# Kernel tuning notes

Hardware: AMD Instinct MI355X
Metric: run time of the kernel (lower is better)

The kernel has to match this reference:

```python
import jax, jax.numpy as jnp
import numpy as np

B, N, D, H = 8, 4096, 1024, 16
HD = D // H
EPS = 1e-5  # torch layer_norm default


def setup_inputs() -> dict:
    key = jax.random.key(0)
    ks = jax.random.split(key, 18)
    s = 1.0 / np.sqrt(D)

    def lin(k):
        return jax.random.normal(k, (D, D), jnp.float32) * s, jnp.zeros((D,), jnp.float32)

    Wg_w, Wg_b = lin(ks[0])
    Wr_w, Wr_b = lin(ks[1])
    Wk_w, Wk_b = lin(ks[2])
    Wv_w, Wv_b = lin(ks[3])
    Wo_w, Wo_b = lin(ks[4])
    mg = jax.random.uniform(ks[5], (D,), jnp.float32)
    mr = jax.random.uniform(ks[6], (D,), jnp.float32)
    mk = jax.random.uniform(ks[7], (D,), jnp.float32)
    mv = jax.random.uniform(ks[8], (D,), jnp.float32)
    w = jax.random.normal(ks[9], (H, HD), jnp.float32)
    u = jax.random.normal(ks[10], (H, HD), jnp.float32)
    x = jax.random.normal(ks[11], (B, N, D), jnp.float32)
    return {"x": x, "Wg_w": Wg_w, "Wg_b": Wg_b, "Wr_w": Wr_w, "Wr_b": Wr_b,
            "Wk_w": Wk_w, "Wk_b": Wk_b, "Wv_w": Wv_w, "Wv_b": Wv_b,
            "Wo_w": Wo_w, "Wo_b": Wo_b, "mg": mg, "mr": mr, "mk": mk, "mv": mv,
            "w": w, "u": u}


def reference(x, Wg_w, Wg_b, Wr_w, Wr_b, Wk_w, Wk_b, Wv_w, Wv_b, Wo_w, Wo_b,
              mg, mr, mk, mv, w, u):
    b, n, d = x.shape
    x_shift = jnp.roll(x, shift=1, axis=1)  # torch.roll wraps: row 0 <- row N-1

    def mix(m, W, bias):
        return (m * x + (1.0 - m) * x_shift) @ W.T + bias

    g = mix(mg, Wg_w, Wg_b).reshape(b, n, H, HD)
    r = mix(mr, Wr_w, Wr_b).reshape(b, n, H, HD)
    k = mix(mk, Wk_w, Wk_b).reshape(b, n, H, HD)
    v = mix(mv, Wv_w, Wv_b).reshape(b, n, H, HD)

    kv = k * v  # [B,N,H,HD]
    decay = jnp.exp(-jnp.exp(w))  # [H,HD]

    # sequential decay scan over time: acc_t = decay*acc_{t-1} + kv_t
    kv_t = jnp.swapaxes(kv, 0, 1)  # [N,B,H,HD]

    def step(acc, kvt):
        acc = decay * acc + kvt
        return acc, acc

    _, accs = jax.lax.scan(step, jnp.zeros((b, H, HD), x.dtype), kv_t)
    wkv = jnp.swapaxes(accs, 0, 1) + u * kv  # [B,N,H,HD]

    rw = r * wkv
    mean = jnp.mean(rw, axis=-1, keepdims=True)
    var = jnp.var(rw, axis=-1, keepdims=True)
    ln = (rw - mean) * jax.lax.rsqrt(var + EPS)

    out = (jax.nn.sigmoid(g) * ln).reshape(b, n, d)
    return out @ Wo_w.T + Wo_b
```

## Files before the change

### kernel.cpp

```cpp
#include <hip/hip_runtime.h>
#include <stdint.h>

#define NB 8
#define NSEQ 4096
#define DMODEL 1024
#define NH 16
#define HDIM 64
#define MROWS (NB*NSEQ)
#define NCHUNK 128
#define CHUNKL (NSEQ/NCHUNK)
#define MIXROWS 16

typedef unsigned short u16;
typedef float f32x4 __attribute__((ext_vector_type(4)));
typedef short bf16x8 __attribute__((ext_vector_type(8)));
typedef unsigned short u16x8 __attribute__((ext_vector_type(8)));

__device__ __forceinline__ u16 f2b(float f) {
  unsigned int u = __builtin_bit_cast(unsigned int, f);
  u = (u + 0x7FFFu + ((u >> 16) & 1u)) >> 16;
  return (u16)u;
}
__device__ __forceinline__ float b2f(u16 s) {
  unsigned int u = ((unsigned int)s) << 16;
  return __builtin_bit_cast(float, u);
}

__device__ __forceinline__ void gload16(const void* g, void* l) {
  __builtin_amdgcn_global_load_lds(
      (const __attribute__((address_space(1))) void*)g,
      (__attribute__((address_space(3))) void*)l, 16, 0, 0);
}

__global__ __launch_bounds__(256) void cvt5(
    const float* __restrict__ a0, const float* __restrict__ a1,
    const float* __restrict__ a2, const float* __restrict__ a3,
    const float* __restrict__ a4,
    u16* __restrict__ b0, u16* __restrict__ b1, u16* __restrict__ b2,
    u16* __restrict__ b3, u16* __restrict__ b4)
{
  const int mat = blockIdx.x >> 7;
  const int blk = blockIdx.x & 127;
  const float* s; u16* d;
  switch (mat) {
    case 0: s = a0; d = b0; break;
    case 1: s = a1; d = b1; break;
    case 2: s = a2; d = b2; break;
    case 3: s = a3; d = b3; break;
    default: s = a4; d = b4; break;
  }
#pragma unroll
  for (int it = 0; it < 8; ++it) {
    const int idx = blk*8192 + it*1024 + threadIdx.x*4;
    const float4 v = *(const float4*)(s + idx);
    ushort4 o; o.x = f2b(v.x); o.y = f2b(v.y); o.z = f2b(v.z); o.w = f2b(v.w);
    *(ushort4*)(d + idx) = o;
  }
}

__global__ __launch_bounds__(256) void mix4_kernel(
    const float* __restrict__ X,
    const float* __restrict__ mg, const float* __restrict__ mr,
    const float* __restrict__ mk, const float* __restrict__ mv,
    u16* __restrict__ Ag, u16* __restrict__ Ar, u16* __restrict__ Ak, u16* __restrict__ Av)
{
  const int g = threadIdx.x >> 7;
  const int t = threadIdx.x & 127;
  const int c8 = t * 8;
  const int r0 = blockIdx.x * MIXROWS + g * (MIXROWS/2);

  float mgv[8], mrv[8], mkv[8], mvv[8];
  *(float4*)&mgv[0] = *(const float4*)(mg + c8); *(float4*)&mgv[4] = *(const float4*)(mg + c8 + 4);
  *(float4*)&mrv[0] = *(const float4*)(mr + c8); *(float4*)&mrv[4] = *(const float4*)(mr + c8 + 4);
  *(float4*)&mkv[0] = *(const float4*)(mk + c8); *(float4*)&mkv[4] = *(const float4*)(mk + c8 + 4);
  *(float4*)&mvv[0] = *(const float4*)(mv + c8); *(float4*)&mvv[4] = *(const float4*)(mv + c8 + 4);

  const int nidx = r0 & (NSEQ-1);
  const int prow = (nidx == 0) ? r0 + (NSEQ-1) : r0 - 1;
  float prev[8];
  *(float4*)&prev[0] = *(const float4*)(X + (size_t)prow*DMODEL + c8);
  *(float4*)&prev[4] = *(const float4*)(X + (size_t)prow*DMODEL + c8 + 4);

#pragma unroll
  for (int j = 0; j < MIXROWS/2; ++j) {
    const size_t o = (size_t)(r0 + j)*DMODEL + c8;
    float cur[8];
    *(float4*)&cur[0] = *(const float4*)(X + o);
    *(float4*)&cur[4] = *(const float4*)(X + o + 4);
#define DO_MIX(MV, AP) { \
      bf16x8 s_; \
      _Pragma("unroll") \
      for (int e = 0; e < 8; ++e) s_[e] = (short)f2b(prev[e] + MV[e]*(cur[e]-prev[e])); \
      *(bf16x8*)(AP + o) = s_; }
    DO_MIX(mgv, Ag)
    DO_MIX(mrv, Ar)
    DO_MIX(mkv, Ak)
    DO_MIX(mvv, Av)
#undef DO_MIX
#pragma unroll
    for (int e = 0; e < 8; ++e) prev[e] = cur[e];
  }
}

#define FENCE asm volatile("" ::: "memory")
#define BAR() { FENCE; __builtin_amdgcn_s_barrier(); FENCE; }
#define PRIO1 __builtin_amdgcn_s_setprio(1)
#define PRIO0 __builtin_amdgcn_s_setprio(0)
#define VM6 asm volatile("s_waitcnt vmcnt(6)" ::: "memory")
#define VM4 asm volatile("s_waitcnt vmcnt(4)" ::: "memory")
#define VM0 asm volatile("s_waitcnt vmcnt(0)" ::: "memory")

template<int OUTBF, int NSEG>
__global__ __launch_bounds__(512, 2) void gemm256(
    const u16* __restrict__ A0, const u16* __restrict__ W0,
    const float* __restrict__ b0, float* __restrict__ oF0, u16* __restrict__ oB0,
    const u16* __restrict__ A1, const u16* __restrict__ W1,
    const float* __restrict__ b1, float* __restrict__ oF1, u16* __restrict__ oB1)
{
  __shared__ __align__(16) char lds[131072];
  const int tid = threadIdx.x;
  const int wave = tid >> 6, lane = tid & 63;
  const int wm = wave >> 2, wn = wave & 3;
  const int rla = lane & 15, kgrp = lane >> 4;

  const int seg = (NSEG == 2) ? (blockIdx.x >> 9) : 0;
  const u16* Abf = (seg == 0) ? A0 : A1;
  const u16* Wb  = (seg == 0) ? W0 : W1;
  const float* bias = (seg == 0) ? b0 : b1;
  float* outF = (seg == 0) ? oF0 : oF1;
  u16*   outB = (seg == 0) ? oB0 : oB1;

  const int wg = blockIdx.x & 511;
  const int xcd = wg & 7, slot = wg >> 3;
  const int by = xcd*16 + (slot >> 2);
  const int bx = slot & 3;

  const int F0 = (wave*2+0)*1024 + lane*16;
  const int F1 = (wave*2+1)*1024 + lane*16;
  const int r0 = F0 >> 6, r1 = F1 >> 6;
  const int c80 = ((F0 >> 4) & 3) ^ ((r0 >> 1) & 3);
  const int c81 = ((F1 >> 4) & 3) ^ ((r1 >> 1) & 3);
  const char* Ab = (const char*)Abf;
  const char* Bbp = (const char*)Wb;
  const unsigned ga0 = (unsigned)by*256*2048 + r0*2048 + c80*16;
  const unsigned ga1 = (unsigned)by*256*2048 + r1*2048 + c81*16;
  const unsigned gb0 = (unsigned)bx*256*2048 + r0*2048 + c80*16;
  const unsigned gb1 = (unsigned)bx*256*2048 + r1*2048 + c81*16;
  const int dst0 = wave*2048;
  const int dst1 = wave*2048 + 1024;

  f32x4 acc[8][4];
#pragma unroll
  for (int i = 0; i < 8; ++i)
#pragma unroll
    for (int j = 0; j < 4; ++j) acc[i][j] = f32x4{0.f,0.f,0.f,0.f};
  bf16x8 af[8], bfr[4];
  const int lane_ds = rla*64 + ((kgrp ^ ((rla>>1)&3)) << 4);

#define LDS_A(D,KK) (lds + (D)*32768 + (KK)*16384)
#define LDS_B(D,KK) (lds + 65536 + (D)*32768 + (KK)*16384)
#define LDA(D,KK) { _Pragma("unroll") for (int mi_ = 0; mi_ < 8; ++mi_) \
    af[mi_] = *(const bf16x8*)(LDS_A(D,KK) + (wm*128 + mi_*16)*64 + lane_ds); }
#define LDB(P,D,KK) { _Pragma("unroll") for (int j_ = 0; j_ < 2; ++j_) \
    bfr[(P)*2+j_] = *(const bf16x8*)(LDS_B(D,KK) + (wn*64 + ((P)*2+j_)*16)*64 + lane_ds); }
#define MM(P) { _Pragma("unroll") for (int mi_ = 0; mi_ < 8; ++mi_) { \
    acc[mi_][(P)*2+0] = __builtin_amdgcn_mfma_f32_16x16x32_bf16(af[mi_], bfr[(P)*2+0], acc[mi_][(P)*2+0], 0,0,0); \
    acc[mi_][(P)*2+1] = __builtin_amdgcn_mfma_f32_16x16x32_bf16(af[mi_], bfr[(P)*2+1], acc[mi_][(P)*2+1], 0,0,0); } }
#define STAGE(ISB, T, KK) { \
    const char* g_ = (ISB) ? Bbp : Ab; \
    const unsigned o0_ = ((ISB) ? gb0 : ga0) + (T)*128 + (KK)*64; \
    const unsigned o1_ = ((ISB) ? gb1 : ga1) + (T)*128 + (KK)*64; \
    char* l_ = (ISB) ? LDS_B((T)&1, KK) : LDS_A((T)&1, KK); \
    gload16(g_ + o0_, l_ + dst0); \
    gload16(g_ + o1_, l_ + dst1); }

  STAGE(0, 0, 0); STAGE(1, 0, 0); STAGE(0, 0, 1); STAGE(1, 0, 1);
  VM4;
  STAGE(0, 1, 0); STAGE(1, 1, 0); STAGE(0, 1, 1);
  VM6;
  BAR();

  for (int i = 0; i < 8; ++i) {
    const int t1 = 2*i+1, t2 = 2*i+2, t3 = 2*i+3;
    const bool s2 = (i < 7);
    LDA(0,0); LDB(0,0,0); STAGE(1, t1, 1);
    BAR(); PRIO1; MM(0); PRIO0; BAR();
    LDB(1,0,0); if (s2) STAGE(0, t2, 0);
    BAR(); PRIO1; MM(1); PRIO0; BAR();
    LDA(0,1); LDB(0,0,1); if (s2) STAGE(1, t2, 0);
    BAR(); PRIO1; MM(0); PRIO0; BAR();
    LDB(1,0,1); if (s2) STAGE(0, t2, 1);
    BAR(); PRIO1; MM(1); PRIO0;
    if (i == 7) { VM0; } else { VM6; }
    BAR();
    LDA(1,0); LDB(0,1,0); if (s2) STAGE(1, t2, 1);
    BAR(); PRIO1; MM(0); PRIO0; BAR();
    LDB(1,1,0); if (s2) STAGE(0, t3, 0);
    BAR(); PRIO1; MM(1); PRIO0; BAR();
    LDA(1,1); LDB(0,1,1); if (s2) STAGE(1, t3, 0);
    BAR(); PRIO1; MM(0); PRIO0; BAR();
    LDB(1,1,1); if (s2) STAGE(0, t3, 1);
    BAR(); PRIO1; MM(1); PRIO0; VM6; BAR();
  }

  float bval[4];
#pragma unroll
  for (int ni = 0; ni < 4; ++ni) bval[ni] = bias[bx*256 + wn*64 + ni*16 + rla];
#pragma unroll
  for (int mi = 0; mi < 8; ++mi) {
    const int gr0 = by*256 + wm*128 + mi*16 + kgrp*4;
    const int gcb = bx*256 + wn*64 + rla;
#pragma unroll
    for (int q = 0; q < 4; ++q) {
      const size_t rowo = (size_t)(gr0 + q)*DMODEL;
#pragma unroll
      for (int ni = 0; ni < 4; ++ni) {
        const float v = acc[mi][ni][q] + bval[ni];
        const size_t o = rowo + gcb + ni*16;
        if (OUTBF) outB[o] = f2b(v);
        else       outF[o] = v;
      }
    }
  }
#undef LDS_A
#undef LDS_B
#undef LDA
#undef LDB
#undef MM
#undef STAGE
}

__global__ __launch_bounds__(128) void scan_pass1(
    const u16* __restrict__ kbuf, const u16* __restrict__ vbuf,
    const float* __restrict__ w, float* __restrict__ chunkAcc)
{
  const int c = blockIdx.x & (NCHUNK-1);
  const int b = blockIdx.x >> 7;
  const int hh = threadIdx.x >> 3;
  const int ch0 = (threadIdx.x & 7) << 3;
  const int hch = hh*HDIM + ch0;

  float dd[8];
#pragma unroll
  for (int j = 0; j < 8; ++j) dd[j] = expf(-expf(w[hch + j]));

  const size_t base = ((size_t)b*NSEQ + (size_t)c*CHUNKL)*DMODEL + hch;
  float acc[8] = {0.f,0.f,0.f,0.f,0.f,0.f,0.f,0.f};
#pragma unroll 2
  for (int i = 0; i < CHUNKL; ++i) {
    const size_t idx = base + (size_t)i*DMODEL;
    const u16x8 k8 = *(const u16x8*)(kbuf + idx);
    const u16x8 v8 = *(const u16x8*)(vbuf + idx);
#pragma unroll
    for (int j = 0; j < 8; ++j)
      acc[j] = dd[j]*acc[j] + b2f(k8[j])*b2f(v8[j]);
  }
  float* cp = &chunkAcc[((size_t)(b*NH + hh)*NCHUNK + c)*HDIM + ch0];
  *(float4*)cp = float4{acc[0], acc[1], acc[2], acc[3]};
  *(float4*)(cp+4) = float4{acc[4], acc[5], acc[6], acc[7]};
}

__global__ __launch_bounds__(64) void scan_pass2(
    const float* __restrict__ chunkAcc, float* __restrict__ carryPrev,
    const float* __restrict__ w)
{
  const int bh = blockIdx.x;
  const int h = bh & (NH-1);
  const int lanehd = threadIdx.x;
  const float e = expf(w[h*HDIM + lanehd]);
  const float dL = expf(-e * (float)CHUNKL);
  const size_t base = (size_t)bh*NCHUNK*HDIM + lanehd;
  float carry = 0.f;
  for (int c = 0; c < NCHUNK; ++c) {
    carryPrev[base + (size_t)c*HDIM] = carry;
    carry = chunkAcc[base + (size_t)c*HDIM] + dL*carry;
  }
}

__global__ __launch_bounds__(128) void scan_pass3(
    const u16* __restrict__ kbuf, const u16* __restrict__ vbuf,
    const u16* __restrict__ rbuf, const u16* __restrict__ gbuf,
    u16* __restrict__ hbuf, const float* __restrict__ carryPrev,
    const float* __restrict__ w, const float* __restrict__ u)
{
  const int c = blockIdx.x & (NCHUNK-1);
  const int b = blockIdx.x >> 7;
  const int hh = threadIdx.x >> 3;
  const int ch0 = (threadIdx.x & 7) << 3;
  const int hch = hh*HDIM + ch0;

  float dd[8], uv[8], carry[8], fac[8], acc[8];
#pragma unroll
  for (int j = 0; j < 8; ++j) {
    dd[j] = expf(-expf(w[hch + j]));
    uv[j] = u[hch + j];
    fac[j] = dd[j];
    acc[j] = 0.f;
  }
  {
    const float* cp = &carryPrev[((size_t)(b*NH + hh)*NCHUNK + c)*HDIM + ch0];
    const float4 c0 = *(const float4*)cp;
    const float4 c1 = *(const float4*)(cp+4);
    carry[0]=c0.x; carry[1]=c0.y; carry[2]=c0.z; carry[3]=c0.w;
    carry[4]=c1.x; carry[5]=c1.y; carry[6]=c1.z; carry[7]=c1.w;
  }

  const size_t base = ((size_t)b*NSEQ + (size_t)c*CHUNKL)*DMODEL + hch;
#pragma unroll 2
  for (int i = 0; i < CHUNKL; ++i) {
    const size_t idx = base + (size_t)i*DMODEL;
    const u16x8 k8 = *(const u16x8*)(kbuf + idx);
    const u16x8 v8 = *(const u16x8*)(vbuf + idx);
    const u16x8 r8 = *(const u16x8*)(rbuf + idx);
    const u16x8 g8 = *(const u16x8*)(gbuf + idx);
    float rw[8];
    float s1 = 0.f, s2 = 0.f;
#pragma unroll
    for (int j = 0; j < 8; ++j) {
      const float kv = b2f(k8[j])*b2f(v8[j]);
      acc[j] = dd[j]*acc[j] + kv;
      const float wkv = acc[j] + fac[j]*carry[j] + uv[j]*kv;
      fac[j] *= dd[j];
      rw[j] = b2f(r8[j])*wkv;
      s1 += rw[j]; s2 += rw[j]*rw[j];
    }
#pragma unroll
    for (int off = 4; off >= 1; off >>= 1) {
      s1 += __shfl_xor(s1, off);
      s2 += __shfl_xor(s2, off);
    }
    const float mean = s1 * (1.f/64.f);
    const float var = s2 * (1.f/64.f) - mean*mean;
    const float rstd = rsqrtf(var + 1e-5f);
    u16x8 o;
#pragma unroll
    for (int j = 0; j < 8; ++j)
      o[j] = f2b((rw[j]-mean)*rstd * (1.f/(1.f+expf(-b2f(g8[j])))));
    *(u16x8*)(hbuf + idx) = o;
  }
}

extern "C" void kernel_launch(void* const* d_in, const int* in_sizes, int n_in,
                              void* d_out, int out_size, void* d_ws, size_t ws_size,
                              hipStream_t stream)
{
  const float* x   = (const float*)d_in[0];
  const float* WgW = (const float*)d_in[1];
  const float* Wgb = (const float*)d_in[2];
  const float* WrW = (const float*)d_in[3];
  const float* Wrb = (const float*)d_in[4];
  const float* WkW = (const float*)d_in[5];
  const float* Wkb = (const float*)d_in[6];
  const float* WvW = (const float*)d_in[7];
  const float* Wvb = (const float*)d_in[8];
  const float* WoW = (const float*)d_in[9];
  const float* Wob = (const float*)d_in[10];
  const float* mg  = (const float*)d_in[11];
  const float* mr  = (const float*)d_in[12];
  const float* mk  = (const float*)d_in[13];
  const float* mv  = (const float*)d_in[14];
  const float* w   = (const float*)d_in[15];
  const float* u   = (const float*)d_in[16];
  char* ws = (char*)d_ws;

  const size_t WBB = (size_t)DMODEL*DMODEL*2;
  u16* WgB = (u16*)(ws + 0*WBB);
  u16* WrB = (u16*)(ws + 1*WBB);
  u16* WkB = (u16*)(ws + 2*WBB);
  u16* WvB = (u16*)(ws + 3*WBB);
  u16* WoB = (u16*)(ws + 4*WBB);
  size_t off = 5*WBB;
  const size_t EL = (size_t)MROWS*DMODEL;

  char* amBase = ws + off;
  u16* Amg = (u16*)(amBase);
  u16* Amr = (u16*)(amBase + EL*2);
  u16* Amk = (u16*)(amBase + EL*4);
  u16* Amv = (u16*)(amBase + EL*6);
  u16* kbuf = Amg;
  u16* vbuf = Amr;
  u16* hbuf = Amk;
  off += EL*8;
  u16* gbuf = (u16*)(ws + off);   off += EL*2;
  u16* rbuf = (u16*)(ws + off);   off += EL*2;
  float* chunkAcc  = (float*)(ws + off); off += (size_t)NB*NH*NCHUNK*HDIM*4;
  float* carryPrev = (float*)(ws + off); off += (size_t)NB*NH*NCHUNK*HDIM*4;

  cvt5<<<640, 256, 0, stream>>>(WgW, WrW, WkW, WvW, WoW, WgB, WrB, WkB, WvB, WoB);

  mix4_kernel<<<MROWS/MIXROWS, 256, 0, stream>>>(x, mg, mr, mk, mv, Amg, Amr, Amk, Amv);

  gemm256<1,2><<<1024, 512, 0, stream>>>(Amg, WgB, Wgb, nullptr, gbuf,
                                         Amr, WrB, Wrb, nullptr, rbuf);
  gemm256<1,2><<<1024, 512, 0, stream>>>(Amk, WkB, Wkb, nullptr, kbuf,
                                         Amv, WvB, Wvb, nullptr, vbuf);

  scan_pass1<<<NB*NCHUNK, 128, 0, stream>>>(kbuf, vbuf, w, chunkAcc);
  scan_pass2<<<NB*NH, 64, 0, stream>>>(chunkAcc, carryPrev, w);
  scan_pass3<<<NB*NCHUNK, 128, 0, stream>>>(kbuf, vbuf, rbuf, gbuf, hbuf, carryPrev, w, u);

  gemm256<0,1><<<512, 512, 0, stream>>>(hbuf, WoB, Wob, (float*)d_out, nullptr,
                                        nullptr, nullptr, nullptr, nullptr, nullptr);
}
```

Before: 552.0 us.

## Loop GEMM blocks over several N tiles and fuse weight conversion with mixing

Each GEMM workgroup now walks TPB consecutive output-column tiles for a fixed row block. The K-loop software pipeline runs continuously across tile boundaries, so the prologue is paid once per block and the grid shrinks to 256 workgroups. The weight bf16 conversion and the token-mix kernel are merged into one launch with a block-index split. The trade-off is only one 512-thread workgroup per CU instead of two resident, which reduces latency hiding. The same A rows are also re-streamed for every column tile.

```diff
diff --git a/kernel.cpp b/kernel.cpp
--- a/kernel.cpp
+++ b/kernel.cpp
@@ -32,38 +32,39 @@
       (__attribute__((address_space(3))) void*)l, 16, 0, 0);
 }
 
-__global__ __launch_bounds__(256) void cvt5(
+__global__ __launch_bounds__(256) void prep_kernel(
+    const float* __restrict__ X,
+    const float* __restrict__ mg, const float* __restrict__ mr,
+    const float* __restrict__ mk, const float* __restrict__ mv,
+    u16* __restrict__ Ag, u16* __restrict__ Ar, u16* __restrict__ Ak, u16* __restrict__ Av,
     const float* __restrict__ a0, const float* __restrict__ a1,
     const float* __restrict__ a2, const float* __restrict__ a3,
     const float* __restrict__ a4,
     u16* __restrict__ b0, u16* __restrict__ b1, u16* __restrict__ b2,
     u16* __restrict__ b3, u16* __restrict__ b4)
 {
-  const int mat = blockIdx.x >> 7;
-  const int blk = blockIdx.x & 127;
-  const float* s; u16* d;
-  switch (mat) {
-    case 0: s = a0; d = b0; break;
-    case 1: s = a1; d = b1; break;
-    case 2: s = a2; d = b2; break;
-    case 3: s = a3; d = b3; break;
-    default: s = a4; d = b4; break;
-  }
-#pragma unroll
-  for (int it = 0; it < 8; ++it) {
-    const int idx = blk*8192 + it*1024 + threadIdx.x*4;
-    const float4 v = *(const float4*)(s + idx);
-    ushort4 o; o.x = f2b(v.x); o.y = f2b(v.y); o.z = f2b(v.z); o.w = f2b(v.w);
-    *(ushort4*)(d + idx) = o;
-  }
-}
-
-__global__ __launch_bounds__(256) void mix4_kernel(
-    const float* __restrict__ X,
-    const float* __restrict__ mg, const float* __restrict__ mr,
-    const float* __restrict__ mk, const float* __restrict__ mv,
-    u16* __restrict__ Ag, u16* __restrict__ Ar, u16* __restrict__ Ak, u16* __restrict__ Av)
-{
+  if (blockIdx.x >= 2048) {
+    const int cb = blockIdx.x - 2048;
+    const int mat = cb >> 7;
+    const int blk = cb & 127;
+    const float* s; u16* d;
+    switch (mat) {
+      case 0: s = a0; d = b0; break;
+      case 1: s = a1; d = b1; break;
+      case 2: s = a2; d = b2; break;
+      case 3: s = a3; d = b3; break;
+      default: s = a4; d = b4; break;
+    }
+#pragma unroll
+    for (int it = 0; it < 8; ++it) {
+      const int idx = blk*8192 + it*1024 + threadIdx.x*4;
+      const float4 v = *(const float4*)(s + idx);
+      ushort4 o; o.x = f2b(v.x); o.y = f2b(v.y); o.z = f2b(v.z); o.w = f2b(v.w);
+      *(ushort4*)(d + idx) = o;
+    }
+    return;
+  }
+
   const int g = threadIdx.x >> 7;
   const int t = threadIdx.x & 127;
   const int c8 = t * 8;
@@ -110,7 +111,7 @@
 #define VM4 asm volatile("s_waitcnt vmcnt(4)" ::: "memory")
 #define VM0 asm volatile("s_waitcnt vmcnt(0)" ::: "memory")
 
-template<int OUTBF, int NSEG>
+template<int OUTBF, int NSEG, int TPB>
 __global__ __launch_bounds__(512, 2) void gemm256(
     const u16* __restrict__ A0, const u16* __restrict__ W0,
     const float* __restrict__ b0, float* __restrict__ oF0, u16* __restrict__ oB0,
@@ -123,17 +124,18 @@
   const int wm = wave >> 2, wn = wave & 3;
   const int rla = lane & 15, kgrp = lane >> 4;
 
-  const int seg = (NSEG == 2) ? (blockIdx.x >> 9) : 0;
+  const int seg = (NSEG == 2) ? ((int)blockIdx.x >> 7) : 0;
+  const int wgl = (NSEG == 2) ? ((int)blockIdx.x & 127) : (int)blockIdx.x;
   const u16* Abf = (seg == 0) ? A0 : A1;
   const u16* Wb  = (seg == 0) ? W0 : W1;
   const float* bias = (seg == 0) ? b0 : b1;
   float* outF = (seg == 0) ? oF0 : oF1;
   u16*   outB = (seg == 0) ? oB0 : oB1;
 
-  const int wg = blockIdx.x & 511;
-  const int xcd = wg & 7, slot = wg >> 3;
-  const int by = xcd*16 + (slot >> 2);
-  const int bx = slot & 3;
+  const int xcd = wgl & 7;
+  const int gidx = wgl >> 3;
+  const int by = xcd*16 + (gidx & 15);
+  const int bxBase = (gidx >> 4) * TPB;
 
   const int F0 = (wave*2+0)*1024 + lane*16;
   const int F1 = (wave*2+1)*1024 + lane*16;
@@ -144,10 +146,17 @@
   const char* Bbp = (const char*)Wb;
   const unsigned ga0 = (unsigned)by*256*2048 + r0*2048 + c80*16;
   const unsigned ga1 = (unsigned)by*256*2048 + r1*2048 + c81*16;
-  const unsigned gb0 = (unsigned)bx*256*2048 + r0*2048 + c80*16;
-  const unsigned gb1 = (unsigned)bx*256*2048 + r1*2048 + c81*16;
+  const unsigned gb0 = (unsigned)bxBase*256*2048 + r0*2048 + c80*16;
+  const unsigned gb1 = (unsigned)bxBase*256*2048 + r1*2048 + c81*16;
   const int dst0 = wave*2048;
   const int dst1 = wave*2048 + 1024;
+
+  float bval[TPB][4];
+#pragma unroll
+  for (int tt = 0; tt < TPB; ++tt)
+#pragma unroll
+    for (int ni = 0; ni < 4; ++ni)
+      bval[tt][ni] = bias[(bxBase+tt)*256 + wn*64 + ni*16 + rla];
 
   f32x4 acc[8][4];
 #pragma unroll
@@ -168,8 +177,10 @@
     acc[mi_][(P)*2+1] = __builtin_amdgcn_mfma_f32_16x16x32_bf16(af[mi_], bfr[(P)*2+1], acc[mi_][(P)*2+1], 0,0,0); } }
 #define STAGE(ISB, T, KK) { \
     const char* g_ = (ISB) ? Bbp : Ab; \
-    const unsigned o0_ = ((ISB) ? gb0 : ga0) + (T)*128 + (KK)*64; \
-    const unsigned o1_ = ((ISB) ? gb1 : ga1) + (T)*128 + (KK)*64; \
+    const unsigned tof_ = (ISB) ? ((unsigned)((T)>>4)*524288u + (unsigned)((T)&15)*128u) \
+                                : ((unsigned)((T)&15)*128u); \
+    const unsigned o0_ = ((ISB) ? gb0 : ga0) + tof_ + (KK)*64; \
+    const unsigned o1_ = ((ISB) ? gb1 : ga1) + tof_ + (KK)*64; \
     char* l_ = (ISB) ? LDS_B((T)&1, KK) : LDS_A((T)&1, KK); \
     gload16(g_ + o0_, l_ + dst0); \
     gload16(g_ + o1_, l_ + dst1); }
@@ -180,45 +191,56 @@
   VM6;
   BAR();
 
-  for (int i = 0; i < 8; ++i) {
-    const int t1 = 2*i+1, t2 = 2*i+2, t3 = 2*i+3;
-    const bool s2 = (i < 7);
-    LDA(0,0); LDB(0,0,0); STAGE(1, t1, 1);
-    BAR(); PRIO1; MM(0); PRIO0; BAR();
-    LDB(1,0,0); if (s2) STAGE(0, t2, 0);
-    BAR(); PRIO1; MM(1); PRIO0; BAR();
-    LDA(0,1); LDB(0,0,1); if (s2) STAGE(1, t2, 0);
-    BAR(); PRIO1; MM(0); PRIO0; BAR();
-    LDB(1,0,1); if (s2) STAGE(0, t2, 1);
-    BAR(); PRIO1; MM(1); PRIO0;
-    if (i == 7) { VM0; } else { VM6; }
-    BAR();
-    LDA(1,0); LDB(0,1,0); if (s2) STAGE(1, t2, 1);
-    BAR(); PRIO1; MM(0); PRIO0; BAR();
-    LDB(1,1,0); if (s2) STAGE(0, t3, 0);
-    BAR(); PRIO1; MM(1); PRIO0; BAR();
-    LDA(1,1); LDB(0,1,1); if (s2) STAGE(1, t3, 0);
-    BAR(); PRIO1; MM(0); PRIO0; BAR();
-    LDB(1,1,1); if (s2) STAGE(0, t3, 1);
-    BAR(); PRIO1; MM(1); PRIO0; VM6; BAR();
-  }
-
-  float bval[4];
-#pragma unroll
-  for (int ni = 0; ni < 4; ++ni) bval[ni] = bias[bx*256 + wn*64 + ni*16 + rla];
-#pragma unroll
-  for (int mi = 0; mi < 8; ++mi) {
-    const int gr0 = by*256 + wm*128 + mi*16 + kgrp*4;
-    const int gcb = bx*256 + wn*64 + rla;
-#pragma unroll
-    for (int q = 0; q < 4; ++q) {
-      const size_t rowo = (size_t)(gr0 + q)*DMODEL;
-#pragma unroll
-      for (int ni = 0; ni < 4; ++ni) {
-        const float v = acc[mi][ni][q] + bval[ni];
-        const size_t o = rowo + gcb + ni*16;
-        if (OUTBF) outB[o] = f2b(v);
-        else       outF[o] = v;
+  const int NT = TPB*16;
+#pragma unroll
+  for (int tile = 0; tile < TPB; ++tile) {
+#pragma unroll 1
+    for (int ii = 0; ii < 8; ++ii) {
+      const int i = tile*8 + ii;
+      const int t1 = 2*i+1, t2 = 2*i+2, t3 = 2*i+3;
+      const bool s2 = (t2 < NT);
+      LDA(0,0); LDB(0,0,0); STAGE(1, t1, 1);
+      BAR(); PRIO1; MM(0); PRIO0; BAR();
+      LDB(1,0,0); if (s2) STAGE(0, t2, 0);
+      BAR(); PRIO1; MM(1); PRIO0; BAR();
+      LDA(0,1); LDB(0,0,1); if (s2) STAGE(1, t2, 0);
+      BAR(); PRIO1; MM(0); PRIO0; BAR();
+      LDB(1,0,1); if (s2) STAGE(0, t2, 1);
+      BAR(); PRIO1; MM(1); PRIO0;
+      if (tile == TPB-1 && ii == 7) { VM0; } else { VM6; }
+      BAR();
+      LDA(1,0); LDB(0,1,0); if (s2) STAGE(1, t2, 1);
+      BAR(); PRIO1; MM(0); PRIO0; BAR();
+      LDB(1,1,0); if (s2) STAGE(0, t3, 0);
+      BAR(); PRIO1; MM(1); PRIO0; BAR();
+      LDA(1,1); LDB(0,1,1); if (s2) STAGE(1, t3, 0);
+      BAR(); PRIO1; MM(0); PRIO0; BAR();
+      LDB(1,1,1); if (s2) STAGE(0, t3, 1);
+      BAR(); PRIO1; MM(1); PRIO0; VM6; BAR();
+    }
+    {
+      const int bx_ = bxBase + tile;
+      const int gcb = bx_*256 + wn*64 + rla;
+#pragma unroll
+      for (int mi = 0; mi < 8; ++mi) {
+        const int gr0_ = by*256 + wm*128 + mi*16 + kgrp*4;
+#pragma unroll
+        for (int q = 0; q < 4; ++q) {
+          const size_t rowo = (size_t)(gr0_ + q)*DMODEL;
+#pragma unroll
+          for (int ni = 0; ni < 4; ++ni) {
+            const float v = acc[mi][ni][q] + bval[tile][ni];
+            const size_t o = rowo + gcb + ni*16;
+            if (OUTBF) outB[o] = f2b(v);
+            else       outF[o] = v;
+          }
+        }
+      }
+      if (tile < TPB-1) {
+#pragma unroll
+        for (int mi = 0; mi < 8; ++mi)
+#pragma unroll
+          for (int ni = 0; ni < 4; ++ni) acc[mi][ni] = f32x4{0.f,0.f,0.f,0.f};
       }
     }
   }
@@ -386,19 +408,19 @@
   float* chunkAcc  = (float*)(ws + off); off += (size_t)NB*NH*NCHUNK*HDIM*4;
   float* carryPrev = (float*)(ws + off); off += (size_t)NB*NH*NCHUNK*HDIM*4;
 
-  cvt5<<<640, 256, 0, stream>>>(WgW, WrW, WkW, WvW, WoW, WgB, WrB, WkB, WvB, WoB);
-
-  mix4_kernel<<<MROWS/MIXROWS, 256, 0, stream>>>(x, mg, mr, mk, mv, Amg, Amr, Amk, Amv);
-
-  gemm256<1,2><<<1024, 512, 0, stream>>>(Amg, WgB, Wgb, nullptr, gbuf,
-                                         Amr, WrB, Wrb, nullptr, rbuf);
-  gemm256<1,2><<<1024, 512, 0, stream>>>(Amk, WkB, Wkb, nullptr, kbuf,
-                                         Amv, WvB, Wvb, nullptr, vbuf);
+  prep_kernel<<<2048 + 640, 256, 0, stream>>>(
+      x, mg, mr, mk, mv, Amg, Amr, Amk, Amv,
+      WgW, WrW, WkW, WvW, WoW, WgB, WrB, WkB, WvB, WoB);
+
+  gemm256<1,2,4><<<256, 512, 0, stream>>>(Amg, WgB, Wgb, nullptr, gbuf,
+                                          Amr, WrB, Wrb, nullptr, rbuf);
+  gemm256<1,2,4><<<256, 512, 0, stream>>>(Amk, WkB, Wkb, nullptr, kbuf,
+                                          Amv, WvB, Wvb, nullptr, vbuf);
 
   scan_pass1<<<NB*NCHUNK, 128, 0, stream>>>(kbuf, vbuf, w, chunkAcc);
   scan_pass2<<<NB*NH, 64, 0, stream>>>(chunkAcc, carryPrev, w);
   scan_pass3<<<NB*NCHUNK, 128, 0, stream>>>(kbuf, vbuf, rbuf, gbuf, hbuf, carryPrev, w, u);
 
-  gemm256<0,1><<<512, 512, 0, stream>>>(hbuf, WoB, Wob, (float*)d_out, nullptr,
-                                        nullptr, nullptr, nullptr, nullptr, nullptr);
-}
+  gemm256<0,1,2><<<256, 512, 0, stream>>>(hbuf, WoB, Wob, (float*)d_out, nullptr,
+                                          nullptr, nullptr, nullptr, nullptr, nullptr);
+}
```

Measured after the change: 582.8 us. 1.06x slower.
